# Optimization experiments

Measured on AMD Instinct MI355X. Metric: run time of the kernel, lower is better.

The kernel has to match this reference:

```python
import jax, jax.numpy as jnp
import numpy as np

D_MODEL = 1024
NUM_HEADS = 16
D_HEAD = D_MODEL // NUM_HEADS
MAX_DISTANCE = 128
SEQ_LEN = 2048


def setup_inputs() -> dict:
    key = jax.random.key(0)
    k_x, k_qkv, k_out, k_bias = jax.random.split(key, 4)
    scale = 1.0 / np.sqrt(D_MODEL)
    return {
        "x": jax.random.normal(k_x, (SEQ_LEN, D_MODEL), dtype=jnp.float32),
        "w_qkv": jax.random.normal(k_qkv, (D_MODEL, 3 * D_MODEL), dtype=jnp.float32) * scale,
        "w_out": jax.random.normal(k_out, (D_MODEL, D_MODEL), dtype=jnp.float32) * scale,
        "rel_bias": jax.random.normal(k_bias, (MAX_DISTANCE, NUM_HEADS), dtype=jnp.float32) * 0.02,
    }


def _position_bias(rel_bias, seq_len):
    # relative_position[q, k] = k - q; bucket = clip(|rel|, 0, max_distance-1)
    ctx = jnp.arange(seq_len)[:, None]
    mem = jnp.arange(seq_len)[None, :]
    bucket = jnp.clip(jnp.abs(mem - ctx), 0, MAX_DISTANCE - 1)  # [q, k]
    return rel_bias[bucket]  # [q, k, h]


def reference(x, w_qkv, w_out, rel_bias):
    seq_len = x.shape[0]
    qkv = x @ w_qkv  # [s, 3*d_model]
    q, k, v = jnp.split(qkv, 3, axis=-1)
    q = q.reshape(seq_len, NUM_HEADS, D_HEAD)
    k = k.reshape(seq_len, NUM_HEADS, D_HEAD)
    v = v.reshape(seq_len, NUM_HEADS, D_HEAD)
    bias = _position_bias(rel_bias, seq_len)  # [q, k, h]
    # flax dot_product_attention semantics: scale q by 1/sqrt(d_head), add bias, softmax over kv
    scores = jnp.einsum("qhd,khd->hqk", q, k) / jnp.sqrt(jnp.asarray(D_HEAD, q.dtype))
    scores = scores + jnp.transpose(bias, (2, 0, 1))  # [h, q, k]
    weights = jax.nn.softmax(scores, axis=-1)
    attn = jnp.einsum("hqk,khd->qhd", weights, v)  # [s, h, d_head]
    attn = attn.reshape(1, seq_len, D_MODEL)
    return attn @ w_out  # [1, s, d_model]
```

## Files before the change

### kernel.cpp

```cpp
#include <hip/hip_runtime.h>
#include <hip/hip_bf16.h>

#define SEQ   2048
#define DM    1024
#define NH    16
#define DH    64
#define MAXD  128

#define LOG2E 1.44269504f

typedef __attribute__((ext_vector_type(8))) short  short8;
typedef __attribute__((ext_vector_type(4))) float  float4v;

__device__ __forceinline__ short8 ld8(const void* p) {
    short8 v; __builtin_memcpy(&v, p, 16); return v;
}
__device__ __forceinline__ void st8(void* p, short8 v) {
    __builtin_memcpy(p, &v, 16);
}
__device__ __forceinline__ short bf16bits(float f) {
    __hip_bfloat16 b = __float2bfloat16(f);
    short s; __builtin_memcpy(&s, &b, 2); return s;
}
__device__ __forceinline__ float bits2f(short s) {
    unsigned u = (unsigned)(unsigned short)s << 16;
    return __builtin_bit_cast(float, u);
}
__device__ __forceinline__ unsigned packbf2(float a, float b) {
    unsigned ua = (__builtin_bit_cast(unsigned, a) + 0x8000u) >> 16;
    unsigned ub = (__builtin_bit_cast(unsigned, b) + 0x8000u) & 0xffff0000u;
    return ua | ub;
}
__device__ __forceinline__ unsigned packh2(float a, float b) {
    _Float16 ha = (_Float16)a, hb = (_Float16)b;
    unsigned short ua, ub;
    __builtin_memcpy(&ua, &ha, 2); __builtin_memcpy(&ub, &hb, 2);
    return (unsigned)ua | ((unsigned)ub << 16);
}
__device__ __forceinline__ float f16tof(short s) {
    _Float16 h; __builtin_memcpy(&h, &s, 2); return (float)h;
}
__device__ __forceinline__ float fexp2(float x) {
    float r; asm("v_exp_f32 %0, %1" : "=v"(r) : "v"(x)); return r;
}

__device__ __forceinline__ void async16(void* lds, const void* g) {
    __builtin_amdgcn_global_load_lds(
        (const __attribute__((address_space(1))) unsigned int*)g,
        (__attribute__((address_space(3))) unsigned int*)lds, 16, 0, 0);
}

__global__ __launch_bounds__(256) void prep_kernel(
    const float* __restrict__ wq, const float* __restrict__ wo,
    const float* __restrict__ x,
    __hip_bfloat16* __restrict__ wqT, __hip_bfloat16* __restrict__ woT,
    __hip_bfloat16* __restrict__ xb) {
    const int t = threadIdx.x;
    const int bx = blockIdx.x;
    if (bx >= 128) {
        const size_t id = (size_t)(bx - 128) * 32 + blockIdx.y;
        const size_t i  = id * 2048 + t * 8;
        float f[8]; __builtin_memcpy(f, x + i, 32);
        short8 v;
#pragma unroll
        for (int j = 0; j < 8; ++j) v[j] = bf16bits(f[j]);
        st8(xb + i, v);
        return;
    }
    __shared__ __hip_bfloat16 tile[32][33];
    const int tx = t % 32, ty = t / 32;
    const int r0 = blockIdx.y * 32;
    const float* src; __hip_bfloat16* dst; int ss, ds, c0;
    if (bx < 96) { src = wq; dst = wqT; ss = 3 * DM; ds = DM; c0 = bx * 32; }
    else         { src = wo; dst = woT; ss = DM;     ds = DM; c0 = (bx - 96) * 32; }
#pragma unroll
    for (int i = 0; i < 4; ++i)
        tile[ty + i * 8][tx] = __float2bfloat16(src[(size_t)(r0 + ty + i * 8) * ss + c0 + tx]);
    __syncthreads();
#pragma unroll
    for (int i = 0; i < 4; ++i)
        dst[(size_t)(c0 + ty + i * 8) * ds + r0 + tx] = tile[tx][ty + i * 8];
}

__global__ __launch_bounds__(256) void gemm_qkv(
    const __hip_bfloat16* __restrict__ A,
    const __hip_bfloat16* __restrict__ BT,
    __hip_bfloat16* __restrict__ C,
    __hip_bfloat16* __restrict__ vTg,
    int M, int N, int K) {
    __shared__ short Smem[2 * 128 * 64];
    short* As = Smem;
    short* Bs = Smem + 128 * 64;

    const int t = threadIdx.x;
    const int w = t >> 6, lane = t & 63;
    const int l15 = lane & 15, quad = lane >> 4;
    const int row0 = blockIdx.y * 128;
    const int col0 = blockIdx.x * 128;
    const int wm = w >> 1, wn = w & 1;

    float4v acc[4][4];
#pragma unroll
    for (int i = 0; i < 4; ++i)
#pragma unroll
        for (int j = 0; j < 4; ++j) acc[i][j] = (float4v){0.f, 0.f, 0.f, 0.f};

    const int rowoff  = w * 8 + (lane >> 3);
    const int lanecol = (((lane & 7) ^ ((lane >> 3) & 7)) << 4);
    const char* ap = (const char*)A  + ((size_t)(row0 + rowoff) * K) * 2 + lanecol;
    const char* bp = (const char*)BT + ((size_t)(col0 + rowoff) * K) * 2 + lanecol;

    const int swr = (l15 & 7) << 4;

    for (int k0 = 0; k0 < K; k0 += 64) {
#pragma unroll
        for (int p = 0; p < 4; ++p)
            async16(&As[p * 2048 + w * 512], ap + (size_t)p * 32 * K * 2 + k0 * 2);
#pragma unroll
        for (int p = 0; p < 4; ++p)
            async16(&Bs[p * 2048 + w * 512], bp + (size_t)p * 32 * K * 2 + k0 * 2);
        __syncthreads();

#pragma unroll
        for (int kc = 0; kc < 2; ++kc) {
            short8 af[4], bf[4];
#pragma unroll
            for (int mt = 0; mt < 4; ++mt) {
                const int ra = wm * 64 + mt * 16 + l15;
                af[mt] = ld8((const char*)As + ra * 128 + ((kc * 64 + quad * 16) ^ swr));
            }
#pragma unroll
            for (int nt = 0; nt < 4; ++nt) {
                const int rb = wn * 64 + nt * 16 + l15;
                bf[nt] = ld8((const char*)Bs + rb * 128 + ((kc * 64 + quad * 16) ^ swr));
            }
#pragma unroll
            for (int mt = 0; mt < 4; ++mt)
#pragma unroll
                for (int nt = 0; nt < 4; ++nt)
                    acc[mt][nt] = __builtin_amdgcn_mfma_f32_16x16x32_bf16(
                        af[mt], bf[nt], acc[mt][nt], 0, 0, 0);
        }
        __syncthreads();
    }

    if (col0 < 2 * DM) {
#pragma unroll
        for (int mt = 0; mt < 4; ++mt)
#pragma unroll
            for (int nt = 0; nt < 4; ++nt)
#pragma unroll
                for (int r = 0; r < 4; ++r) {
                    const int row = row0 + wm * 64 + mt * 16 + quad * 4 + r;
                    const int col = col0 + wn * 64 + nt * 16 + l15;
                    C[(size_t)row * N + col] = __float2bfloat16(acc[mt][nt][r]);
                }
    } else {
        short* Tv = Smem;
#pragma unroll
        for (int H = 0; H < 2; ++H) {
            if (wn == H) {
#pragma unroll
                for (int mt = 0; mt < 4; ++mt)
#pragma unroll
                    for (int nt = 0; nt < 4; ++nt)
#pragma unroll
                        for (int r = 0; r < 4; ++r)
                            Tv[(nt * 16 + l15) * 132 + wm * 64 + mt * 16 + quad * 4 + r] =
                                bf16bits(acc[mt][nt][r]);
            }
            __syncthreads();
#pragma unroll
            for (int p = 0; p < 4; ++p) {
                const int idx = p * 256 + t;
                const int dl = idx >> 4, uu = idx & 15;
                st8(&vTg[((size_t)(col0 - 2 * DM) + H * 64 + dl) * SEQ + row0 + uu * 8],
                    ld8(&Tv[dl * 132 + uu * 8]));
            }
            __syncthreads();
        }
    }
}

__global__ __launch_bounds__(256) void gemm_out(
    const __hip_bfloat16* __restrict__ A,
    const __hip_bfloat16* __restrict__ BT,
    float* __restrict__ C,
    int M, int N, int K) {
    __shared__ short As[64 * 64];
    __shared__ short Bs[64 * 64];

    const int t = threadIdx.x;
    const int w = t >> 6, lane = t & 63;
    const int l15 = lane & 15, quad = lane >> 4;
    const int row0 = blockIdx.y * 64;
    const int col0 = blockIdx.x * 64;
    const int wm = w >> 1, wn = w & 1;

    float4v acc[2][2];
#pragma unroll
    for (int i = 0; i < 2; ++i)
#pragma unroll
        for (int j = 0; j < 2; ++j) acc[i][j] = (float4v){0.f, 0.f, 0.f, 0.f};

    const int rowoff  = w * 8 + (lane >> 3);
    const int lanecol = (((lane & 7) ^ ((lane >> 3) & 7)) << 4);
    const char* ap = (const char*)A  + ((size_t)(row0 + rowoff) * K) * 2 + lanecol;
    const char* bp = (const char*)BT + ((size_t)(col0 + rowoff) * K) * 2 + lanecol;

    const int swr = (l15 & 7) << 4;

    for (int k0 = 0; k0 < K; k0 += 64) {
#pragma unroll
        for (int r = 0; r < 2; ++r)
            async16(&As[r * 2048 + w * 512], ap + (size_t)r * 32 * K * 2 + k0 * 2);
#pragma unroll
        for (int r = 0; r < 2; ++r)
            async16(&Bs[r * 2048 + w * 512], bp + (size_t)r * 32 * K * 2 + k0 * 2);
        __syncthreads();

#pragma unroll
        for (int kc = 0; kc < 2; ++kc) {
            short8 af[2], bf[2];
#pragma unroll
            for (int mt = 0; mt < 2; ++mt) {
                const int ra = wm * 32 + mt * 16 + l15;
                af[mt] = ld8((const char*)As + ra * 128 + ((kc * 64 + quad * 16) ^ swr));
            }
#pragma unroll
            for (int nt = 0; nt < 2; ++nt) {
                const int rb = wn * 32 + nt * 16 + l15;
                bf[nt] = ld8((const char*)Bs + rb * 128 + ((kc * 64 + quad * 16) ^ swr));
            }
#pragma unroll
            for (int mt = 0; mt < 2; ++mt)
#pragma unroll
                for (int nt = 0; nt < 2; ++nt)
                    acc[mt][nt] = __builtin_amdgcn_mfma_f32_16x16x32_bf16(
                        af[mt], bf[nt], acc[mt][nt], 0, 0, 0);
        }
        __syncthreads();
    }

#pragma unroll
    for (int mt = 0; mt < 2; ++mt)
#pragma unroll
        for (int nt = 0; nt < 2; ++nt)
#pragma unroll
            for (int r = 0; r < 4; ++r) {
                const int row = row0 + wm * 32 + mt * 16 + quad * 4 + r;
                const int col = col0 + wn * 32 + nt * 16 + l15;
                C[(size_t)row * N + col] = acc[mt][nt][r];
            }
}

#define TK    128
#define NTILE (SEQ / 2 / TK)
#define KS    68
#define VS    132
#define PS    140

__global__ __launch_bounds__(256, 2) void attn_part(
    const __hip_bfloat16* __restrict__ qkv,
    const __hip_bfloat16* __restrict__ vT,
    const float* __restrict__ rel_bias,
    short* __restrict__ opart,
    float* __restrict__ ml) {
    __shared__ short KtP[4 * 32 * PS];
    __shared__ short Vt[DH * VS];
    __shared__ float biasL[MAXD];

    const int t = threadIdx.x;
    const int w = t >> 6, lane = t & 63;
    const int l15 = lane & 15, quad = lane >> 4;

    const int id = blockIdx.x;
    const int qb = (id >> 3) & 15;
    const int c  = (id & 7) + 8 * (id >> 7);
    const int h  = c & 15;
    const int half = c >> 4;
    const int kbase = half * (SEQ / 2);
    const int qw = qb * 128 + w * 32;

    if (t < MAXD) biasL[t] = rel_bias[t * NH + h] * LOG2E;

    short8 qf[2][2];
#pragma unroll
    for (int qg = 0; qg < 2; ++qg)
#pragma unroll
        for (int cc = 0; cc < 2; ++cc) {
            short8 raw = ld8(qkv + (size_t)(qw + qg * 16 + l15) * (3 * DM) + h * DH + cc * 32 + quad * 8);
#pragma unroll
            for (int j = 0; j < 8; ++j) qf[qg][cc][j] = bf16bits(bits2f(raw[j]) * (0.125f * LOG2E));
        }

    float4v o_acc[4][2];
#pragma unroll
    for (int nt = 0; nt < 4; ++nt)
#pragma unroll
        for (int qg = 0; qg < 2; ++qg) o_acc[nt][qg] = (float4v){0.f, 0.f, 0.f, 0.f};
    float m_i[2] = {-1e30f, -1e30f}, l_i[2] = {0.f, 0.f};

    short* Pw = &KtP[w * 32 * PS];

    for (int kb = 0; kb < NTILE; ++kb) {
        const int k0 = kbase + kb * TK;
#pragma unroll
        for (int p = 0; p < 4; ++p) {
            const int idx = p * 256 + t;
            const int row = idx >> 3, u = idx & 7;
            st8(&KtP[row * KS + u * 8],
                ld8(qkv + (size_t)(k0 + row) * (3 * DM) + DM + h * DH + u * 8));
        }
#pragma unroll
        for (int p = 0; p < 4; ++p) {
            const int idx = p * 256 + t;
            const int row = idx >> 4, u = idx & 15;
            st8(&Vt[row * VS + u * 8],
                ld8(vT + (size_t)(h * DH + row) * SEQ + k0 + u * 8));
        }
        __syncthreads();

        float4v s_acc[2][8];
#pragma unroll
        for (int qg = 0; qg < 2; ++qg)
#pragma unroll
            for (int kt = 0; kt < 8; ++kt) s_acc[qg][kt] = (float4v){0.f, 0.f, 0.f, 0.f};
#pragma unroll
        for (int cc = 0; cc < 2; ++cc)
#pragma unroll
            for (int kt = 0; kt < 8; ++kt) {
                short8 kf = ld8(&KtP[(kt * 16 + l15) * KS + (cc * 4 + quad) * 8]);
                s_acc[0][kt] = __builtin_amdgcn_mfma_f32_16x16x32_bf16(kf, qf[0][cc], s_acc[0][kt], 0, 0, 0);
                s_acc[1][kt] = __builtin_amdgcn_mfma_f32_16x16x32_bf16(kf, qf[1][cc], s_acc[1][kt], 0, 0, 0);
            }

        const int dlo = k0 - (qw + 31);
        const int dhi = qw - (k0 + TK - 1);
        if (dlo >= MAXD - 1 || dhi >= MAXD - 1) {
            const float bu = biasL[MAXD - 1];
#pragma unroll
            for (int qg = 0; qg < 2; ++qg)
#pragma unroll
                for (int kt = 0; kt < 8; ++kt)
#pragma unroll
                    for (int r = 0; r < 4; ++r) s_acc[qg][kt][r] += bu;
        } else {
#pragma unroll
            for (int qg = 0; qg < 2; ++qg) {
                const int qrow = qw + qg * 16 + l15;
#pragma unroll
                for (int kt = 0; kt < 8; ++kt)
#pragma unroll
                    for (int r = 0; r < 4; ++r) {
                        const int kg = k0 + kt * 16 + quad * 4 + r;
                        int rel = kg - qrow; if (rel < 0) rel = -rel;
                        if (rel > MAXD - 1) rel = MAXD - 1;
                        s_acc[qg][kt][r] += biasL[rel];
                    }
            }
        }

        float al[2];
#pragma unroll
        for (int qg = 0; qg < 2; ++qg) {
            float mk[8];
#pragma unroll
            for (int kt = 0; kt < 8; ++kt)
                mk[kt] = fmaxf(fmaxf(s_acc[qg][kt][0], s_acc[qg][kt][1]),
                               fmaxf(s_acc[qg][kt][2], s_acc[qg][kt][3]));
            float m = fmaxf(fmaxf(fmaxf(mk[0], mk[1]), fmaxf(mk[2], mk[3])),
                            fmaxf(fmaxf(mk[4], mk[5]), fmaxf(mk[6], mk[7])));
            m = fmaxf(m, __shfl_xor(m, 16, 64));
            m = fmaxf(m, __shfl_xor(m, 32, 64));
            const float mn = fmaxf(m_i[qg], m);
            al[qg] = fexp2(m_i[qg] - mn);
            m_i[qg] = mn;
            float sk[8];
#pragma unroll
            for (int kt = 0; kt < 8; ++kt) {
                float p0 = fexp2(s_acc[qg][kt][0] - mn);
                float p1 = fexp2(s_acc[qg][kt][1] - mn);
                float p2 = fexp2(s_acc[qg][kt][2] - mn);
                float p3 = fexp2(s_acc[qg][kt][3] - mn);
                s_acc[qg][kt][0] = p0; s_acc[qg][kt][1] = p1;
                s_acc[qg][kt][2] = p2; s_acc[qg][kt][3] = p3;
                sk[kt] = (p0 + p1) + (p2 + p3);
            }
            float rs = ((sk[0] + sk[1]) + (sk[2] + sk[3])) +
                       ((sk[4] + sk[5]) + (sk[6] + sk[7]));
            rs += __shfl_xor(rs, 16, 64);
            rs += __shfl_xor(rs, 32, 64);
            l_i[qg] = l_i[qg] * al[qg] + rs;
        }
#pragma unroll
        for (int nt = 0; nt < 4; ++nt)
#pragma unroll
            for (int qg = 0; qg < 2; ++qg)
#pragma unroll
                for (int r = 0; r < 4; ++r) o_acc[nt][qg][r] *= al[qg];

        __syncthreads();

#pragma unroll
        for (int qg = 0; qg < 2; ++qg)
#pragma unroll
            for (int kt = 0; kt < 8; ++kt) {
                unsigned d0 = packbf2(s_acc[qg][kt][0], s_acc[qg][kt][1]);
                unsigned d1 = packbf2(s_acc[qg][kt][2], s_acc[qg][kt][3]);
                unsigned long long v = (unsigned long long)d0 | ((unsigned long long)d1 << 32);
                __builtin_memcpy(&Pw[(qg * 16 + l15) * PS + kt * 16 + quad * 4], &v, 8);
            }

#pragma unroll
        for (int kc = 0; kc < 4; ++kc) {
            short8 pf0 = ld8(&Pw[l15 * PS + kc * 32 + quad * 8]);
            short8 pf1 = ld8(&Pw[(16 + l15) * PS + kc * 32 + quad * 8]);
#pragma unroll
            for (int nt = 0; nt < 4; ++nt) {
                short8 vf = ld8(&Vt[(nt * 16 + l15) * VS + kc * 32 + quad * 8]);
                o_acc[nt][0] = __builtin_amdgcn_mfma_f32_16x16x32_bf16(vf, pf0, o_acc[nt][0], 0, 0, 0);
                o_acc[nt][1] = __builtin_amdgcn_mfma_f32_16x16x32_bf16(vf, pf1, o_acc[nt][1], 0, 0, 0);
            }
        }
        __syncthreads();
    }

#pragma unroll
    for (int qg = 0; qg < 2; ++qg) {
        const float inv = 1.f / l_i[qg];
        const int qrow = qw + qg * 16 + l15;
#pragma unroll
        for (int nt = 0; nt < 4; ++nt) {
            unsigned d0 = packh2(o_acc[nt][qg][0] * inv, o_acc[nt][qg][1] * inv);
            unsigned d1 = packh2(o_acc[nt][qg][2] * inv, o_acc[nt][qg][3] * inv);
            unsigned long long v = (unsigned long long)d0 | ((unsigned long long)d1 << 32);
            __builtin_memcpy(opart + ((size_t)half * SEQ + qrow) * DM + h * DH + nt * 16 + quad * 4, &v, 8);
        }
    }
    if (quad == 0) {
#pragma unroll
        for (int qg = 0; qg < 2; ++qg) {
            const int qrow = qw + qg * 16 + l15;
            float* mp = ml + (((size_t)half * SEQ + qrow) * NH + h) * 2;
            mp[0] = m_i[qg];
            mp[1] = l_i[qg];
        }
    }
}

__global__ __launch_bounds__(256) void combine_kernel(
    const short* __restrict__ opart,
    const float* __restrict__ ml,
    __hip_bfloat16* __restrict__ attnb) {
    const size_t e = ((size_t)blockIdx.x * 256 + threadIdx.x) * 8;
    const int row = (int)(e >> 10);
    const int c0  = (int)(e & 1023);
    const int h   = c0 >> 6;

    const float* mp1 = ml + ((size_t)row * NH + h) * 2;
    const float* mp2 = mp1 + (size_t)SEQ * NH * 2;
    const float m1 = mp1[0], l1 = mp1[1];
    const float m2 = mp2[0], l2 = mp2[1];
    const float mx = fmaxf(m1, m2);
    const float e1 = fexp2(m1 - mx) * l1;
    const float e2 = fexp2(m2 - mx) * l2;
    const float inv = 1.f / (e1 + e2);
    const float w1 = e1 * inv, w2 = e2 * inv;

    short8 a = ld8(opart + (size_t)row * DM + c0);
    short8 b = ld8(opart + (size_t)SEQ * DM + (size_t)row * DM + c0);
    short8 o;
#pragma unroll
    for (int j = 0; j < 8; ++j)
        o[j] = bf16bits(w1 * f16tof(a[j]) + w2 * f16tof(b[j]));
    st8(attnb + (size_t)row * DM + c0, o);
}

extern "C" void kernel_launch(void* const* d_in, const int* in_sizes, int n_in,
                              void* d_out, int out_size, void* d_ws, size_t ws_size,
                              hipStream_t stream) {
    const float* x        = (const float*)d_in[0];
    const float* w_qkv    = (const float*)d_in[1];
    const float* w_out    = (const float*)d_in[2];
    const float* rel_bias = (const float*)d_in[3];
    float* out = (float*)d_out;

    char* p = (char*)d_ws;
    __hip_bfloat16* xb    = (__hip_bfloat16*)p;  p += (size_t)SEQ * DM * 2;
    __hip_bfloat16* wqT   = (__hip_bfloat16*)p;  p += (size_t)3 * DM * DM * 2;
    __hip_bfloat16* woT   = (__hip_bfloat16*)p;  p += (size_t)DM * DM * 2;
    __hip_bfloat16* qkvb  = (__hip_bfloat16*)p;  p += (size_t)SEQ * 3 * DM * 2;
    __hip_bfloat16* vT    = (__hip_bfloat16*)p;  p += (size_t)DM * SEQ * 2;
    __hip_bfloat16* attnb = (__hip_bfloat16*)p;

    short* opart = (short*)d_ws;
    float* ml    = (float*)((char*)d_ws + (size_t)2 * SEQ * DM * 2);

    prep_kernel<<<dim3(160, 32), 256, 0, stream>>>(w_qkv, w_out, x, wqT, woT, xb);

    gemm_qkv<<<dim3(3 * DM / 128, SEQ / 128), 256, 0, stream>>>(
        xb, wqT, qkvb, vT, SEQ, 3 * DM, DM);

    attn_part<<<512, 256, 0, stream>>>(qkvb, vT, rel_bias, opart, ml);
    combine_kernel<<<1024, 256, 0, stream>>>(opart, ml, attnb);

    gemm_out<<<dim3(DM / 64, SEQ / 64), 256, 0, stream>>>(
        attnb, woT, out, SEQ, DM, DM);
}
```

Measured before the change: 153.2 us.

## Split attention KV into four parts and load K/V fragments directly from global

The attention kernel now splits the key range into four partitions instead of two, doubling the grid to 1024 blocks, and raises the occupancy hint to 4 blocks per CU. K and V tiles are no longer staged through shared memory; each lane loads its MFMA fragments straight from global memory, which removes the per-tile barriers and frees LDS for higher occupancy. Partial outputs for parts 2-3 are stored in the output buffer as scratch before the final GEMM overwrites it, and the combine kernel merges four partials. The trade-off is uncoalesced, cache-dependent global fragment loads and more combine traffic.

```diff
diff --git a/kernel.cpp b/kernel.cpp
--- a/kernel.cpp
+++ b/kernel.cpp
@@ -255,19 +255,18 @@
 }
 
 #define TK    128
-#define NTILE (SEQ / 2 / TK)
-#define KS    68
-#define VS    132
+#define NTT   (SEQ / TK)
+#define NPART 4
 #define PS    140
 
-__global__ __launch_bounds__(256, 2) void attn_part(
+__global__ __launch_bounds__(256, 4) void attn_part(
     const __hip_bfloat16* __restrict__ qkv,
     const __hip_bfloat16* __restrict__ vT,
     const float* __restrict__ rel_bias,
-    short* __restrict__ opart,
+    short* __restrict__ opart01,
+    short* __restrict__ opart23,
     float* __restrict__ ml) {
-    __shared__ short KtP[4 * 32 * PS];
-    __shared__ short Vt[DH * VS];
+    __shared__ short Pl[4][32 * PS];
     __shared__ float biasL[MAXD];
 
     const int t = threadIdx.x;
@@ -278,11 +277,13 @@
     const int qb = (id >> 3) & 15;
     const int c  = (id & 7) + 8 * (id >> 7);
     const int h  = c & 15;
-    const int half = c >> 4;
-    const int kbase = half * (SEQ / 2);
+    const int part = c >> 4;
+    const int kb_lo = part * (NTT / NPART);
+    const int kb_hi = kb_lo + (NTT / NPART);
     const int qw = qb * 128 + w * 32;
 
     if (t < MAXD) biasL[t] = rel_bias[t * NH + h] * LOG2E;
+    __syncthreads();
 
     short8 qf[2][2];
 #pragma unroll
@@ -301,36 +302,25 @@
         for (int qg = 0; qg < 2; ++qg) o_acc[nt][qg] = (float4v){0.f, 0.f, 0.f, 0.f};
     float m_i[2] = {-1e30f, -1e30f}, l_i[2] = {0.f, 0.f};
 
-    short* Pw = &KtP[w * 32 * PS];
-
-    for (int kb = 0; kb < NTILE; ++kb) {
-        const int k0 = kbase + kb * TK;
-#pragma unroll
-        for (int p = 0; p < 4; ++p) {
-            const int idx = p * 256 + t;
-            const int row = idx >> 3, u = idx & 7;
-            st8(&KtP[row * KS + u * 8],
-                ld8(qkv + (size_t)(k0 + row) * (3 * DM) + DM + h * DH + u * 8));
-        }
-#pragma unroll
-        for (int p = 0; p < 4; ++p) {
-            const int idx = p * 256 + t;
-            const int row = idx >> 4, u = idx & 15;
-            st8(&Vt[row * VS + u * 8],
-                ld8(vT + (size_t)(h * DH + row) * SEQ + k0 + u * 8));
-        }
-        __syncthreads();
+    short* Pw = Pl[w];
+
+    const __hip_bfloat16* kbp = qkv + (size_t)l15 * (3 * DM) + DM + h * DH + quad * 8;
+    const __hip_bfloat16* vbp = vT + (size_t)(h * DH + l15) * SEQ + quad * 8;
+
+    for (int kb = kb_lo; kb < kb_hi; ++kb) {
+        const int k0 = kb * TK;
 
         float4v s_acc[2][8];
 #pragma unroll
         for (int qg = 0; qg < 2; ++qg)
 #pragma unroll
             for (int kt = 0; kt < 8; ++kt) s_acc[qg][kt] = (float4v){0.f, 0.f, 0.f, 0.f};
+        const __hip_bfloat16* kt0 = kbp + (size_t)k0 * (3 * DM);
 #pragma unroll
         for (int cc = 0; cc < 2; ++cc)
 #pragma unroll
             for (int kt = 0; kt < 8; ++kt) {
-                short8 kf = ld8(&KtP[(kt * 16 + l15) * KS + (cc * 4 + quad) * 8]);
+                short8 kf = ld8(kt0 + (size_t)(kt * 16) * (3 * DM) + cc * 32);
                 s_acc[0][kt] = __builtin_amdgcn_mfma_f32_16x16x32_bf16(kf, qf[0][cc], s_acc[0][kt], 0, 0, 0);
                 s_acc[1][kt] = __builtin_amdgcn_mfma_f32_16x16x32_bf16(kf, qf[1][cc], s_acc[1][kt], 0, 0, 0);
             }
@@ -400,8 +390,6 @@
 #pragma unroll
                 for (int r = 0; r < 4; ++r) o_acc[nt][qg][r] *= al[qg];
 
-        __syncthreads();
-
 #pragma unroll
         for (int qg = 0; qg < 2; ++qg)
 #pragma unroll
@@ -412,20 +400,22 @@
                 __builtin_memcpy(&Pw[(qg * 16 + l15) * PS + kt * 16 + quad * 4], &v, 8);
             }
 
+        const __hip_bfloat16* vt0 = vbp + k0;
 #pragma unroll
         for (int kc = 0; kc < 4; ++kc) {
             short8 pf0 = ld8(&Pw[l15 * PS + kc * 32 + quad * 8]);
             short8 pf1 = ld8(&Pw[(16 + l15) * PS + kc * 32 + quad * 8]);
 #pragma unroll
             for (int nt = 0; nt < 4; ++nt) {
-                short8 vf = ld8(&Vt[(nt * 16 + l15) * VS + kc * 32 + quad * 8]);
+                short8 vf = ld8(vt0 + (size_t)(nt * 16) * SEQ + kc * 32);
                 o_acc[nt][0] = __builtin_amdgcn_mfma_f32_16x16x32_bf16(vf, pf0, o_acc[nt][0], 0, 0, 0);
                 o_acc[nt][1] = __builtin_amdgcn_mfma_f32_16x16x32_bf16(vf, pf1, o_acc[nt][1], 0, 0, 0);
             }
         }
-        __syncthreads();
-    }
-
+    }
+
+    short* opb = (part < 2) ? (opart01 + (size_t)part * SEQ * DM)
+                            : (opart23 + (size_t)(part - 2) * SEQ * DM);
 #pragma unroll
     for (int qg = 0; qg < 2; ++qg) {
         const float inv = 1.f / l_i[qg];
@@ -435,14 +425,14 @@
             unsigned d0 = packh2(o_acc[nt][qg][0] * inv, o_acc[nt][qg][1] * inv);
             unsigned d1 = packh2(o_acc[nt][qg][2] * inv, o_acc[nt][qg][3] * inv);
             unsigned long long v = (unsigned long long)d0 | ((unsigned long long)d1 << 32);
-            __builtin_memcpy(opart + ((size_t)half * SEQ + qrow) * DM + h * DH + nt * 16 + quad * 4, &v, 8);
+            __builtin_memcpy(opb + (size_t)qrow * DM + h * DH + nt * 16 + quad * 4, &v, 8);
         }
     }
     if (quad == 0) {
 #pragma unroll
         for (int qg = 0; qg < 2; ++qg) {
             const int qrow = qw + qg * 16 + l15;
-            float* mp = ml + (((size_t)half * SEQ + qrow) * NH + h) * 2;
+            float* mp = ml + (((size_t)part * SEQ + qrow) * NH + h) * 2;
             mp[0] = m_i[qg];
             mp[1] = l_i[qg];
         }
@@ -450,7 +440,8 @@
 }
 
 __global__ __launch_bounds__(256) void combine_kernel(
-    const short* __restrict__ opart,
+    const short* __restrict__ opart01,
+    const short* __restrict__ opart23,
     const float* __restrict__ ml,
     __hip_bfloat16* __restrict__ attnb) {
     const size_t e = ((size_t)blockIdx.x * 256 + threadIdx.x) * 8;
@@ -458,22 +449,31 @@
     const int c0  = (int)(e & 1023);
     const int h   = c0 >> 6;
 
-    const float* mp1 = ml + ((size_t)row * NH + h) * 2;
+    const float* mp0 = ml + ((size_t)row * NH + h) * 2;
+    const float* mp1 = mp0 + (size_t)SEQ * NH * 2;
     const float* mp2 = mp1 + (size_t)SEQ * NH * 2;
+    const float* mp3 = mp2 + (size_t)SEQ * NH * 2;
+    const float m0 = mp0[0], l0 = mp0[1];
     const float m1 = mp1[0], l1 = mp1[1];
     const float m2 = mp2[0], l2 = mp2[1];
-    const float mx = fmaxf(m1, m2);
+    const float m3 = mp3[0], l3 = mp3[1];
+    const float mx = fmaxf(fmaxf(m0, m1), fmaxf(m2, m3));
+    const float e0 = fexp2(m0 - mx) * l0;
     const float e1 = fexp2(m1 - mx) * l1;
     const float e2 = fexp2(m2 - mx) * l2;
-    const float inv = 1.f / (e1 + e2);
-    const float w1 = e1 * inv, w2 = e2 * inv;
-
-    short8 a = ld8(opart + (size_t)row * DM + c0);
-    short8 b = ld8(opart + (size_t)SEQ * DM + (size_t)row * DM + c0);
+    const float e3 = fexp2(m3 - mx) * l3;
+    const float inv = 1.f / (e0 + e1 + e2 + e3);
+    const float w0 = e0 * inv, w1 = e1 * inv, w2 = e2 * inv, w3 = e3 * inv;
+
+    short8 a = ld8(opart01 + (size_t)row * DM + c0);
+    short8 b = ld8(opart01 + (size_t)SEQ * DM + (size_t)row * DM + c0);
+    short8 cc = ld8(opart23 + (size_t)row * DM + c0);
+    short8 d = ld8(opart23 + (size_t)SEQ * DM + (size_t)row * DM + c0);
     short8 o;
 #pragma unroll
     for (int j = 0; j < 8; ++j)
-        o[j] = bf16bits(w1 * f16tof(a[j]) + w2 * f16tof(b[j]));
+        o[j] = bf16bits(w0 * f16tof(a[j]) + w1 * f16tof(b[j]) +
+                        w2 * f16tof(cc[j]) + w3 * f16tof(d[j]));
     st8(attnb + (size_t)row * DM + c0, o);
 }
 
@@ -494,16 +494,17 @@
     __hip_bfloat16* vT    = (__hip_bfloat16*)p;  p += (size_t)DM * SEQ * 2;
     __hip_bfloat16* attnb = (__hip_bfloat16*)p;
 
-    short* opart = (short*)d_ws;
-    float* ml    = (float*)((char*)d_ws + (size_t)2 * SEQ * DM * 2);
+    short* opart01 = (short*)d_ws;
+    float* ml      = (float*)((char*)d_ws + ((size_t)8 << 20));
+    short* opart23 = (short*)d_out;
 
     prep_kernel<<<dim3(160, 32), 256, 0, stream>>>(w_qkv, w_out, x, wqT, woT, xb);
 
     gemm_qkv<<<dim3(3 * DM / 128, SEQ / 128), 256, 0, stream>>>(
         xb, wqT, qkvb, vT, SEQ, 3 * DM, DM);
 
-    attn_part<<<512, 256, 0, stream>>>(qkvb, vT, rel_bias, opart, ml);
-    combine_kernel<<<1024, 256, 0, stream>>>(opart, ml, attnb);
+    attn_part<<<1024, 256, 0, stream>>>(qkvb, vT, rel_bias, opart01, opart23, ml);
+    combine_kernel<<<1024, 256, 0, stream>>>(opart01, opart23, ml, attnb);
 
     gemm_out<<<dim3(DM / 64, SEQ / 64), 256, 0, stream>>>(
         attnb, woT, out, SEQ, DM, DM);
```

Result: slower. 259.9 us (+69.6%).

## Load K/V tiles directly into swizzled LDS and drop a barrier

Applied to the files above, without the earlier changes.

The attention kernel now loads K and V tiles with direct global-to-LDS 16-byte asynchronous copies (async16) instead of staging them through registers. The padded LDS layouts are replaced by unpadded tiles with an XOR swizzle, and per-thread source pointers are precomputed once before the loop. P gets its own LDS buffer instead of aliasing the K tile, which removes one __syncthreads per iteration. In exchange the kernel uses more LDS, and correctness depends on async16 completing its copies before the barrier.

```diff
diff --git a/kernel.cpp b/kernel.cpp
--- a/kernel.cpp
+++ b/kernel.cpp
@@ -256,8 +256,6 @@
 
 #define TK    128
 #define NTILE (SEQ / 2 / TK)
-#define KS    68
-#define VS    132
 #define PS    140
 
 __global__ __launch_bounds__(256, 2) void attn_part(
@@ -266,8 +264,9 @@
     const float* __restrict__ rel_bias,
     short* __restrict__ opart,
     float* __restrict__ ml) {
-    __shared__ short KtP[4 * 32 * PS];
-    __shared__ short Vt[DH * VS];
+    __shared__ short Kt[TK * 64];
+    __shared__ short Vt[DH * TK];
+    __shared__ short Pl[4][32 * PS];
     __shared__ float biasL[MAXD];
 
     const int t = threadIdx.x;
@@ -294,6 +293,21 @@
             for (int j = 0; j < 8; ++j) qf[qg][cc][j] = bf16bits(bits2f(raw[j]) * (0.125f * LOG2E));
         }
 
+    const char* kp[4]; const char* vp[4];
+    {
+        const char* kqb = (const char*)qkv + (size_t)(DM + h * DH) * 2;
+        const char* vqb = (const char*)vT  + (size_t)(h * DH) * SEQ * 2;
+#pragma unroll
+        for (int p = 0; p < 4; ++p) {
+            const int rowK = p * 32 + w * 8 + (lane >> 3);
+            const int colK = ((lane & 7) * 16) ^ ((rowK & 7) << 4);
+            kp[p] = kqb + (size_t)rowK * (3 * DM * 2) + colK;
+            const int rowV = p * 16 + w * 4 + quad;
+            const int colV = (l15 * 16) ^ ((rowV & 7) << 4);
+            vp[p] = vqb + (size_t)rowV * (SEQ * 2) + colV;
+        }
+    }
+
     float4v o_acc[4][2];
 #pragma unroll
     for (int nt = 0; nt < 4; ++nt)
@@ -301,24 +315,17 @@
         for (int qg = 0; qg < 2; ++qg) o_acc[nt][qg] = (float4v){0.f, 0.f, 0.f, 0.f};
     float m_i[2] = {-1e30f, -1e30f}, l_i[2] = {0.f, 0.f};
 
-    short* Pw = &KtP[w * 32 * PS];
+    short* Pw = Pl[w];
+    const int swr = (l15 & 7) << 4;
 
     for (int kb = 0; kb < NTILE; ++kb) {
         const int k0 = kbase + kb * TK;
 #pragma unroll
-        for (int p = 0; p < 4; ++p) {
-            const int idx = p * 256 + t;
-            const int row = idx >> 3, u = idx & 7;
-            st8(&KtP[row * KS + u * 8],
-                ld8(qkv + (size_t)(k0 + row) * (3 * DM) + DM + h * DH + u * 8));
-        }
-#pragma unroll
-        for (int p = 0; p < 4; ++p) {
-            const int idx = p * 256 + t;
-            const int row = idx >> 4, u = idx & 15;
-            st8(&Vt[row * VS + u * 8],
-                ld8(vT + (size_t)(h * DH + row) * SEQ + k0 + u * 8));
-        }
+        for (int p = 0; p < 4; ++p)
+            async16(&Kt[p * 2048 + w * 512], kp[p] + (size_t)k0 * (3 * DM * 2));
+#pragma unroll
+        for (int p = 0; p < 4; ++p)
+            async16(&Vt[p * 2048 + w * 512], vp[p] + k0 * 2);
         __syncthreads();
 
         float4v s_acc[2][8];
@@ -330,7 +337,7 @@
         for (int cc = 0; cc < 2; ++cc)
 #pragma unroll
             for (int kt = 0; kt < 8; ++kt) {
-                short8 kf = ld8(&KtP[(kt * 16 + l15) * KS + (cc * 4 + quad) * 8]);
+                short8 kf = ld8((const char*)Kt + (kt * 16 + l15) * 128 + ((cc * 64 + quad * 16) ^ swr));
                 s_acc[0][kt] = __builtin_amdgcn_mfma_f32_16x16x32_bf16(kf, qf[0][cc], s_acc[0][kt], 0, 0, 0);
                 s_acc[1][kt] = __builtin_amdgcn_mfma_f32_16x16x32_bf16(kf, qf[1][cc], s_acc[1][kt], 0, 0, 0);
             }
@@ -400,8 +407,6 @@
 #pragma unroll
                 for (int r = 0; r < 4; ++r) o_acc[nt][qg][r] *= al[qg];
 
-        __syncthreads();
-
 #pragma unroll
         for (int qg = 0; qg < 2; ++qg)
 #pragma unroll
@@ -418,11 +423,12 @@
             short8 pf1 = ld8(&Pw[(16 + l15) * PS + kc * 32 + quad * 8]);
 #pragma unroll
             for (int nt = 0; nt < 4; ++nt) {
-                short8 vf = ld8(&Vt[(nt * 16 + l15) * VS + kc * 32 + quad * 8]);
+                short8 vf = ld8((const char*)Vt + (nt * 16 + l15) * 256 + ((kc * 64 + quad * 16) ^ swr));
                 o_acc[nt][0] = __builtin_amdgcn_mfma_f32_16x16x32_bf16(vf, pf0, o_acc[nt][0], 0, 0, 0);
                 o_acc[nt][1] = __builtin_amdgcn_mfma_f32_16x16x32_bf16(vf, pf1, o_acc[nt][1], 0, 0, 0);
             }
         }
+
         __syncthreads();
     }
 
```

New measurement: 152.2 us. Within noise of the previous version (-0.7%).
